# Optimization experiments

Measured on AMD Instinct MI355X. Metric: run time of the kernel, lower is better.

## Reference

```python
import jax, jax.numpy as jnp
import numpy as np

V = 30000
Y = 30000
D = 768
B = 8
N = 512
PAD_ID = 0
POS_EXPONENT = 1
NEG_INF = 1e12
LN_EPS = 1e-5


def setup_inputs() -> dict:
    key = jax.random.key(0)
    k1, k2, k3, k4, k5 = jax.random.split(key, 5)
    M_s = jax.random.randint(k1, (B, N), 0, V, dtype=jnp.int64)
    E_v = jax.random.normal(k2, (V, D), dtype=jnp.float32) * 0.02
    E_y = jax.random.normal(k3, (Y, D), dtype=jnp.float32) * 0.02
    # padding_idx=0 -> zero rows
    E_v = E_v.at[PAD_ID].set(0.0)
    E_y = E_y.at[PAD_ID].set(0.0)
    W_A = jax.random.normal(k4, (D, D), dtype=jnp.float32) * (1.0 / np.sqrt(D))
    W_O = jax.random.normal(k5, (D, D), dtype=jnp.float32) * (1.0 / np.sqrt(D))
    gamma = jnp.ones((D,), dtype=jnp.float32)
    beta = jnp.zeros((D,), dtype=jnp.float32)
    return {"M_s": M_s, "E_v": E_v, "E_y": E_y, "W_A": W_A, "W_O": W_O,
            "gamma": gamma, "beta": beta}


def positional_rep(seq_len: int, exponent: int) -> jnp.ndarray:
    idx = jnp.arange(seq_len)
    rel = (idx[None, :] - idx[:, None]).astype(jnp.float32)  # [N, N], j - i
    sign = jnp.where(rel >= 0, 1.0, -1.0)
    return sign * jnp.abs(rel) ** exponent


def layer_norm(x, gamma, beta):
    mu = jnp.mean(x, axis=-1, keepdims=True)
    var = jnp.mean((x - mu) ** 2, axis=-1, keepdims=True)
    return (x - mu) * jax.lax.rsqrt(var + LN_EPS) * gamma + beta


def reference(M_s, E_v, E_y, W_A, W_O, gamma, beta):
    # Embedding lookup (dropout is identity at eval / p=0)
    X = E_v[M_s]                                   # [B, N, D]
    Q = X                                          # self-attention mode (v_q=None)
    mask = (M_s != PAD_ID)                         # [B, N]

    # attention: logits = (Q @ W_A) @ X^T + pos_bias, mask, softmax
    logits = jnp.einsum('bnd,bmd->bnm', Q @ W_A, X)  # [B, N, N]
    logits = logits + positional_rep(X.shape[1], POS_EXPONENT)[None]
    logits = jnp.where(mask[:, None, :], logits, -NEG_INF)
    A = jax.nn.softmax(logits, axis=-1)            # [B, N, N]
    Q_c = jnp.einsum('bnm,bmd->bnd', A, X @ W_O)   # [B, N, D]

    H = layer_norm(Q_c + Q, gamma, beta)           # [B, N, D]
    y_logits = jnp.einsum('bnd,yd->bny', H, E_y)   # [B, N, Y]
    return y_logits, A
```

## Files before the change

### kernel.cpp

```cpp
#include <hip/hip_runtime.h>
#include <hip/hip_bf16.h>

using bf16 = __hip_bfloat16;
typedef __attribute__((ext_vector_type(8))) short bf16x8;
typedef __attribute__((ext_vector_type(4))) float f32x4;

#define DEV __device__ __forceinline__

#define AS1 __attribute__((address_space(1)))
#define AS3 __attribute__((address_space(3)))
#define SB  __builtin_amdgcn_sched_barrier(0)
#define BARR __builtin_amdgcn_s_barrier()
#define LG0 asm volatile("s_waitcnt lgkmcnt(0)" ::: "memory")
#define VM4 asm volatile("s_waitcnt vmcnt(4)" ::: "memory")
#define VM0 asm volatile("s_waitcnt vmcnt(0)" ::: "memory")

static constexpr int Bsz = 8, Nseq = 512, Dm = 768, Vv = 30000, Yv = 30000;
static constexpr int Ypad = 30208;
static constexpr int Tok = Bsz * Nseq;
static constexpr int NT = Dm / 64;

#define MF16(MQ, NQ)                                                          \
    __builtin_amdgcn_s_setprio(1);                                            \
    _Pragma("unroll") for (int mm = 0; mm < 4; ++mm)                          \
    _Pragma("unroll") for (int nn = 0; nn < 2; ++nn) {                        \
        acc[(MQ)*4+mm][(NQ)*2+nn] = __builtin_amdgcn_mfma_f32_16x16x32_bf16(  \
            afr[mm][0], bfr[nn][0], acc[(MQ)*4+mm][(NQ)*2+nn], 0, 0, 0);      \
        acc[(MQ)*4+mm][(NQ)*2+nn] = __builtin_amdgcn_mfma_f32_16x16x32_bf16(  \
            afr[mm][1], bfr[nn][1], acc[(MQ)*4+mm][(NQ)*2+nn], 0, 0, 0);      \
    }                                                                         \
    __builtin_amdgcn_s_setprio(0);

__global__ __launch_bounds__(512, 2)
void gemm_big(const bf16* __restrict__ Ag, const bf16* __restrict__ Bg,
              float* __restrict__ Cg)
{
    __shared__ bf16 sm[8][8192];

    int bid = blockIdx.x;
    { int cpx = gridDim.x >> 3; bid = (bid & 7) * cpx + (bid >> 3); }
    const int mTile = bid & 15;
    const int nTile = bid >> 4;

    const int tid  = threadIdx.x;
    const int lane = tid & 63;
    const int wid  = tid >> 6;
    const int wm   = wid >> 2;
    const int wn   = wid & 3;

    const int lr = tid >> 3;
    const int sc = ((tid & 7) ^ (lr & 7)) << 3;
    const bf16* aS = Ag + (long)(mTile * 256 + lr) * Dm + sc;
    const bf16* bS = Bg + (long)(nTile * 256 + lr) * Dm + sc;
    const int ldsOff = wid << 9;

    auto stage = [&](int ci, int op, int h, int tile) {
        const bf16* s = (op ? bS : aS) + (long)h * 128 * Dm + tile * 64;
        __builtin_amdgcn_global_load_lds((const AS1 void*)s,
            (AS3 void*)&sm[ci][ldsOff], 16, 0, 0);
        __builtin_amdgcn_global_load_lds((const AS1 void*)(s + (long)64 * Dm),
            (AS3 void*)&sm[ci][4096 + ldsOff], 16, 0, 0);
    };

    const int fl = lane & 15;
    const int fh = lane >> 4;
    const int e0 = (fh ^ (fl & 7)) << 3;
    const int aro = (wm * 64 + fl) * 64;
    const int bro = (wn * 32 + fl) * 64;

    f32x4 acc[8][4] = {};
    bf16x8 afr[4][2], bfr[2][2];

    auto rdA = [&](int ci) {
#pragma unroll
        for (int mm = 0; mm < 4; ++mm) {
            afr[mm][0] = *(const bf16x8*)&sm[ci][aro + mm * 1024 + e0];
            afr[mm][1] = *(const bf16x8*)&sm[ci][aro + mm * 1024 + (e0 ^ 32)];
        }
    };
    auto rdB = [&](int ci) {
#pragma unroll
        for (int nn = 0; nn < 2; ++nn) {
            bfr[nn][0] = *(const bf16x8*)&sm[ci][bro + nn * 1024 + e0];
            bfr[nn][1] = *(const bf16x8*)&sm[ci][bro + nn * 1024 + (e0 ^ 32)];
        }
    };

    stage(0, 0, 0, 0); stage(2, 1, 0, 0); stage(3, 1, 1, 0); stage(1, 0, 1, 0);
    stage(4, 0, 0, 1); stage(7, 1, 1, 1);
    VM4; SB; BARR; SB;

#pragma unroll 1
    for (int t = 0; t < NT - 2; t += 2) {
        stage(6, 1, 0, t + 1);
        rdA(0); rdB(2);
        SB; BARR; LG0; SB;
        MF16(0, 0)
        SB; BARR; SB;
        stage(5, 0, 1, t + 1);
        rdB(3);
        SB; BARR; LG0; SB;
        MF16(0, 1)
        SB; BARR; SB;
        stage(0, 0, 0, t + 2);
        rdA(1);
        SB; BARR; LG0; SB;
        MF16(1, 1)
        SB; BARR; SB;
        stage(3, 1, 1, t + 2);
        rdB(2);
        SB; BARR; LG0; SB;
        MF16(1, 0)
        VM4;
        SB; BARR; SB;
        stage(2, 1, 0, t + 2);
        rdA(4); rdB(6);
        SB; BARR; LG0; SB;
        MF16(0, 0)
        SB; BARR; SB;
        stage(1, 0, 1, t + 2);
        rdB(7);
        SB; BARR; LG0; SB;
        MF16(0, 1)
        SB; BARR; SB;
        stage(4, 0, 0, t + 3);
        rdA(5);
        SB; BARR; LG0; SB;
        MF16(1, 1)
        SB; BARR; SB;
        stage(7, 1, 1, t + 3);
        rdB(6);
        SB; BARR; LG0; SB;
        MF16(1, 0)
        VM4;
        SB; BARR; SB;
    }

    {
        const int t = NT - 2;
        stage(6, 1, 0, t + 1);
        rdA(0); rdB(2);
        SB; BARR; LG0; SB;
        MF16(0, 0)
        SB; BARR; SB;
        stage(5, 0, 1, t + 1);
        rdB(3);
        SB; BARR; LG0; SB;
        MF16(0, 1)
        SB; BARR; SB;
        rdA(1);
        SB; BARR; LG0; SB;
        MF16(1, 1)
        SB; BARR; SB;
        rdB(2);
        SB; BARR; LG0; SB;
        MF16(1, 0)
        VM0;
        SB; BARR; SB;
        rdA(4); rdB(6);
        SB; BARR; LG0; SB;
        MF16(0, 0)
        SB; BARR; SB;
        rdB(7);
        SB; BARR; LG0; SB;
        MF16(0, 1)
        SB; BARR; SB;
        rdA(5);
        SB; BARR; LG0; SB;
        MF16(1, 1)
        SB; BARR; SB;
        rdB(6);
        SB; BARR; LG0; SB;
        MF16(1, 0)
    }

    const int rB = mTile * 256 + wm * 64 + fh * 4;
    const int cB = nTile * 256 + wn * 32 + fl;
#pragma unroll
    for (int mq = 0; mq < 2; ++mq)
#pragma unroll
    for (int mm = 0; mm < 4; ++mm)
#pragma unroll
    for (int nq = 0; nq < 2; ++nq)
#pragma unroll
    for (int nn = 0; nn < 2; ++nn) {
        const int c = cB + nq * 128 + nn * 16;
        if (c >= Yv) continue;
        const int r = rB + mq * 128 + mm * 16;
#pragma unroll
        for (int j = 0; j < 4; ++j)
            Cg[(long)(r + j) * Yv + c] = acc[mq * 4 + mm][nq * 2 + nn][j];
    }
}

template<bool STORE_BF16>
__global__ __launch_bounds__(256)
void gemm_bt(const bf16* __restrict__ Ag, const bf16* __restrict__ Bg,
             void* __restrict__ Cg, int M, int Nc, int K, int ldc,
             long sA, long sB, long sC)
{
    __shared__ bf16 As[128 * 32];
    __shared__ bf16 Bs[128 * 32];

    const int bz = blockIdx.z;
    const bf16* A  = Ag + (long)bz * sA;
    const bf16* Bm = Bg + (long)bz * sB;

    const int bid = blockIdx.x;
    const int nTilesM = M >> 7;
    const int mTile = bid % nTilesM;
    const int nTile = bid / nTilesM;

    const int tid  = threadIdx.x;
    const int wave = tid >> 6;
    const int lane = tid & 63;

    const int sRow = (wave << 4) + (lane >> 2);
    const int sCol = (lane & 3) << 3;

    const long aBase = (long)(mTile * 128) * K;
    const long bBase = (long)(nTile * 128) * K;

    const int fl = lane & 15;
    const int fh = lane >> 4;
    const int wRow = (wave >> 1) << 6;
    const int wCol = (wave & 1) << 6;

    f32x4 acc[4][4] = {};

    for (int k0 = 0; k0 < K; k0 += 32) {
#pragma unroll
        for (int t = 0; t < 2; ++t) {
            const bf16* gA = A  + aBase + (long)(t * 64 + sRow) * K + (k0 + sCol);
            const bf16* gB = Bm + bBase + (long)(t * 64 + sRow) * K + (k0 + sCol);
            bf16* lA = &As[(t * 64 + (wave << 4)) * 32];
            bf16* lB = &Bs[(t * 64 + (wave << 4)) * 32];
            __builtin_amdgcn_global_load_lds(
                (const AS1 void*)gA, (AS3 void*)lA, 16, 0, 0);
            __builtin_amdgcn_global_load_lds(
                (const AS1 void*)gB, (AS3 void*)lB, 16, 0, 0);
        }
        __syncthreads();

        bf16x8 af[4], bfg[4];
#pragma unroll
        for (int m = 0; m < 4; ++m)
            af[m] = *(const bf16x8*)&As[(wRow + m * 16 + fl) * 32 + fh * 8];
#pragma unroll
        for (int n = 0; n < 4; ++n)
            bfg[n] = *(const bf16x8*)&Bs[(wCol + n * 16 + fl) * 32 + fh * 8];
#pragma unroll
        for (int m = 0; m < 4; ++m)
#pragma unroll
            for (int n = 0; n < 4; ++n)
                acc[m][n] = __builtin_amdgcn_mfma_f32_16x16x32_bf16(
                    af[m], bfg[n], acc[m][n], 0, 0, 0);
        __syncthreads();
    }

    const int rBase = mTile * 128 + wRow + fh * 4;
    const int cBase = nTile * 128 + wCol + fl;
#pragma unroll
    for (int m = 0; m < 4; ++m) {
#pragma unroll
        for (int n = 0; n < 4; ++n) {
            int gc = cBase + n * 16;
            int gr = rBase + m * 16;
            if (STORE_BF16) {
                bf16* C = (bf16*)Cg + (long)bz * sC;
#pragma unroll
                for (int j = 0; j < 4; ++j)
                    C[(long)(gr + j) * ldc + gc] = __float2bfloat16(acc[m][n][j]);
            } else {
                float* C = (float*)Cg + (long)bz * sC;
#pragma unroll
                for (int j = 0; j < 4; ++j)
                    C[(long)(gr + j) * ldc + gc] = acc[m][n][j];
            }
        }
    }
}

__global__ __launch_bounds__(192) void k_cvt_ey(const float* __restrict__ Ey,
                                                bf16* __restrict__ Eyb)
{
    int row = blockIdx.x;
    int d = threadIdx.x * 4;
    union { bf16 h[4]; uint2 u; } pk;
    if (row < Yv) {
        float4 v = *(const float4*)(Ey + (long)row * Dm + d);
        pk.h[0] = __float2bfloat16(v.x); pk.h[1] = __float2bfloat16(v.y);
        pk.h[2] = __float2bfloat16(v.z); pk.h[3] = __float2bfloat16(v.w);
    } else {
        pk.h[0] = pk.h[1] = pk.h[2] = pk.h[3] = __float2bfloat16(0.f);
    }
    *(uint2*)(Eyb + (long)row * Dm + d) = pk.u;
}

__global__ void k_wT(const float* __restrict__ WA, const float* __restrict__ WO,
                     bf16* __restrict__ WAT, bf16* __restrict__ WOT)
{
    __shared__ float t[32][33];
    const float* W = blockIdx.z ? WO : WA;
    bf16* WT = blockIdx.z ? WOT : WAT;
    int bx = blockIdx.x * 32;
    int by = blockIdx.y * 32;
    int tx = threadIdx.x, ty = threadIdx.y;
#pragma unroll
    for (int i = 0; i < 32; i += 8)
        t[ty + i][tx] = W[(long)(bx + ty + i) * Dm + (by + tx)];
    __syncthreads();
#pragma unroll
    for (int i = 0; i < 32; i += 8)
        WT[(long)(by + ty + i) * Dm + (bx + tx)] = __float2bfloat16(t[tx][ty + i]);
}

__global__ __launch_bounds__(192) void k_gather(const int* __restrict__ Ms,
                                                const float* __restrict__ Ev,
                                                bf16* __restrict__ Xb)
{
    int token = blockIdx.x;
    int id = Ms[token];
    int d = threadIdx.x * 4;
    float4 v = *(const float4*)(Ev + (long)id * Dm + d);
    union { bf16 h[4]; uint2 u; } pk;
    pk.h[0] = __float2bfloat16(v.x); pk.h[1] = __float2bfloat16(v.y);
    pk.h[2] = __float2bfloat16(v.z); pk.h[3] = __float2bfloat16(v.w);
    *(uint2*)(Xb + (long)token * Dm + d) = pk.u;
}

__global__ void k_xwoT(const bf16* __restrict__ Xo, bf16* __restrict__ XoT)
{
    __shared__ bf16 t[32][33];
    int b = blockIdx.z;
    const bf16* src = Xo + (long)b * Nseq * Dm;
    bf16* dst = XoT + (long)b * Dm * Nseq;
    int bx = blockIdx.x * 32;
    int by = blockIdx.y * 32;
    int tx = threadIdx.x, ty = threadIdx.y;
#pragma unroll
    for (int i = 0; i < 32; i += 8)
        t[ty + i][tx] = src[(long)(bx + ty + i) * Dm + (by + tx)];
    __syncthreads();
#pragma unroll
    for (int i = 0; i < 32; i += 8)
        dst[(long)(by + ty + i) * Nseq + (bx + tx)] = t[tx][ty + i];
}

DEV float waveMax(float v) {
#pragma unroll
    for (int o = 32; o > 0; o >>= 1) v = fmaxf(v, __shfl_xor(v, o, 64));
    return v;
}
DEV float waveSum(float v) {
#pragma unroll
    for (int o = 32; o > 0; o >>= 1) v += __shfl_xor(v, o, 64);
    return v;
}

__global__ __launch_bounds__(256) void k_softmax(const float* __restrict__ L,
                                                 const int* __restrict__ Ms,
                                                 float* __restrict__ Aout,
                                                 bf16* __restrict__ Ab)
{
    __shared__ float red[8];
    int row = blockIdx.x;
    int b = row >> 9, i = row & 511;
    const float* l = L + (long)row * Nseq;
    const int* ms = Ms + (b << 9);
    int t = threadIdx.x;
    int wid = t >> 6, lane = t & 63;
    int j0 = t, j1 = t + 256;

    float a0 = l[j0] + (float)(j0 - i);
    float a1 = l[j1] + (float)(j1 - i);
    if (ms[j0] == 0) a0 = -1e12f;
    if (ms[j1] == 0) a1 = -1e12f;

    float m = waveMax(fmaxf(a0, a1));
    if (lane == 0) red[wid] = m;
    __syncthreads();
    m = fmaxf(fmaxf(red[0], red[1]), fmaxf(red[2], red[3]));

    float e0 = expf(a0 - m), e1 = expf(a1 - m);
    float s = waveSum(e0 + e1);
    if (lane == 0) red[4 + wid] = s;
    __syncthreads();
    s = red[4] + red[5] + red[6] + red[7];
    float inv = 1.0f / s;

    float r0 = e0 * inv, r1 = e1 * inv;
    Aout[(long)row * Nseq + j0] = r0;
    Aout[(long)row * Nseq + j1] = r1;
    Ab[(long)row * Nseq + j0] = __float2bfloat16(r0);
    Ab[(long)row * Nseq + j1] = __float2bfloat16(r1);
}

__global__ __launch_bounds__(256) void k_ln(const float* __restrict__ Qc,
                                            const int* __restrict__ Ms,
                                            const float* __restrict__ Ev,
                                            const float* __restrict__ gamma,
                                            const float* __restrict__ beta,
                                            bf16* __restrict__ Hb)
{
    __shared__ float red[8];
    int row = blockIdx.x;
    int id = Ms[row];
    const float* q = Qc + (long)row * Dm;
    const float* e = Ev + (long)id * Dm;
    int t = threadIdx.x;
    int wid = t >> 6, lane = t & 63;

    float x[3];
#pragma unroll
    for (int c = 0; c < 3; ++c) x[c] = q[t + c * 256] + e[t + c * 256];

    float s = waveSum(x[0] + x[1] + x[2]);
    if (lane == 0) red[wid] = s;
    __syncthreads();
    float mu = (red[0] + red[1] + red[2] + red[3]) * (1.0f / 768.0f);

    float vs = 0.f;
#pragma unroll
    for (int c = 0; c < 3; ++c) { float d = x[c] - mu; vs += d * d; }
    vs = waveSum(vs);
    if (lane == 0) red[4 + wid] = vs;
    __syncthreads();
    float var = (red[4] + red[5] + red[6] + red[7]) * (1.0f / 768.0f);
    float rstd = rsqrtf(var + 1e-5f);

#pragma unroll
    for (int c = 0; c < 3; ++c) {
        int d = t + c * 256;
        Hb[(long)row * Dm + d] =
            __float2bfloat16((x[c] - mu) * rstd * gamma[d] + beta[d]);
    }
}

extern "C" void kernel_launch(void* const* d_in, const int* in_sizes, int n_in,
                              void* d_out, int out_size, void* d_ws, size_t ws_size,
                              hipStream_t stream)
{
    const int*   Ms    = (const int*)d_in[0];
    const float* Ev    = (const float*)d_in[1];
    const float* Ey    = (const float*)d_in[2];
    const float* WA    = (const float*)d_in[3];
    const float* WO    = (const float*)d_in[4];
    const float* gamma = (const float*)d_in[5];
    const float* beta  = (const float*)d_in[6];

    float* y_out = (float*)d_out;
    float* A_out = y_out + (size_t)Tok * Yv;

    char* ws = (char*)d_ws;
    size_t off = 0;
    auto alloc = [&](size_t n) { char* p = ws + off; off += (n + 255) & ~(size_t)255; return p; };
    bf16*  Xb    = (bf16*) alloc((size_t)Tok * Dm * 2);
    bf16*  WAbT  = (bf16*) alloc((size_t)Dm * Dm * 2);
    bf16*  WObT  = (bf16*) alloc((size_t)Dm * Dm * 2);
    bf16*  QWb   = (bf16*) alloc((size_t)Tok * Dm * 2);
    bf16*  XWob  = (bf16*) alloc((size_t)Tok * Dm * 2);
    bf16*  XWobT = (bf16*) alloc((size_t)Tok * Dm * 2);
    float* Lf    = (float*)alloc((size_t)Tok * Nseq * 4);
    bf16*  Ab    = (bf16*) alloc((size_t)Tok * Nseq * 2);
    float* Qc    = (float*)alloc((size_t)Tok * Dm * 4);
    bf16*  Hb    = (bf16*) alloc((size_t)Tok * Dm * 2);
    bf16*  Eyb   = (bf16*) alloc((size_t)Ypad * Dm * 2);

    k_cvt_ey<<<dim3(Ypad), dim3(192), 0, stream>>>(Ey, Eyb);
    k_wT<<<dim3(24, 24, 2), dim3(32, 8), 0, stream>>>(WA, WO, WAbT, WObT);
    k_gather<<<dim3(Tok), dim3(192), 0, stream>>>(Ms, Ev, Xb);
    gemm_bt<true><<<dim3(192), dim3(256), 0, stream>>>(
        Xb, WAbT, (void*)QWb, Tok, Dm, Dm, Dm, 0L, 0L, 0L);
    gemm_bt<true><<<dim3(192), dim3(256), 0, stream>>>(
        Xb, WObT, (void*)XWob, Tok, Dm, Dm, Dm, 0L, 0L, 0L);
    gemm_bt<false><<<dim3(16, 1, 8), dim3(256), 0, stream>>>(
        QWb, Xb, (void*)Lf, Nseq, Nseq, Dm, Nseq,
        (long)Nseq * Dm, (long)Nseq * Dm, (long)Nseq * Nseq);
    k_softmax<<<dim3(Tok), dim3(256), 0, stream>>>(Lf, Ms, A_out, Ab);
    k_xwoT<<<dim3(16, 24, 8), dim3(32, 8), 0, stream>>>(XWob, XWobT);
    gemm_bt<false><<<dim3(24, 1, 8), dim3(256), 0, stream>>>(
        Ab, XWobT, (void*)Qc, Nseq, Dm, Nseq, Dm,
        (long)Nseq * Nseq, (long)Dm * Nseq, (long)Nseq * Dm);
    k_ln<<<dim3(Tok), dim3(256), 0, stream>>>(Qc, Ms, Ev, gamma, beta, Hb);
    gemm_big<<<dim3(16 * (Ypad / 256)), dim3(512), 0, stream>>>(Hb, Eyb, y_out);
}
```

Before: 391.4 us.

## Make vocab GEMM persistent over N-tiles, double-buffer B fragments, fuse projection GEMMs

The large output GEMM now launches 256 persistent blocks. Each block keeps one M tile and loops over N tiles with a stride of 16, instead of launching one block per tile. It uses two B fragment register sets, so the fourth MFMA group reuses already-loaded B data and skips an LDS read. The two D×D projection GEMMs are merged into one GEMM against a concatenated weight matrix, and downstream kernels read the result through a new lda stride. This removes per-block launch and tail overhead plus a kernel launch, at the cost of more registers and possible load imbalance from the 118/16 tile split.

```diff
diff --git a/kernel.cpp b/kernel.cpp
--- a/kernel.cpp
+++ b/kernel.cpp
@@ -17,17 +17,18 @@
 
 static constexpr int Bsz = 8, Nseq = 512, Dm = 768, Vv = 30000, Yv = 30000;
 static constexpr int Ypad = 30208;
+static constexpr int NTILE = 118;
 static constexpr int Tok = Bsz * Nseq;
 static constexpr int NT = Dm / 64;
 
-#define MF16(MQ, NQ)                                                          \
+#define MF16(MQ, NQ, BR)                                                      \
     __builtin_amdgcn_s_setprio(1);                                            \
     _Pragma("unroll") for (int mm = 0; mm < 4; ++mm)                          \
     _Pragma("unroll") for (int nn = 0; nn < 2; ++nn) {                        \
         acc[(MQ)*4+mm][(NQ)*2+nn] = __builtin_amdgcn_mfma_f32_16x16x32_bf16(  \
-            afr[mm][0], bfr[nn][0], acc[(MQ)*4+mm][(NQ)*2+nn], 0, 0, 0);      \
+            afr[mm][0], BR[nn][0], acc[(MQ)*4+mm][(NQ)*2+nn], 0, 0, 0);       \
         acc[(MQ)*4+mm][(NQ)*2+nn] = __builtin_amdgcn_mfma_f32_16x16x32_bf16(  \
-            afr[mm][1], bfr[nn][1], acc[(MQ)*4+mm][(NQ)*2+nn], 0, 0, 0);      \
+            afr[mm][1], BR[nn][1], acc[(MQ)*4+mm][(NQ)*2+nn], 0, 0, 0);       \
     }                                                                         \
     __builtin_amdgcn_s_setprio(0);
 
@@ -37,10 +38,9 @@
 {
     __shared__ bf16 sm[8][8192];
 
-    int bid = blockIdx.x;
-    { int cpx = gridDim.x >> 3; bid = (bid & 7) * cpx + (bid >> 3); }
-    const int mTile = bid & 15;
-    const int nTile = bid >> 4;
+    const int b = blockIdx.x;
+    const int mTile = b >> 4;
+    const int sIdx  = b & 15;
 
     const int tid  = threadIdx.x;
     const int lane = tid & 63;
@@ -51,16 +51,7 @@
     const int lr = tid >> 3;
     const int sc = ((tid & 7) ^ (lr & 7)) << 3;
     const bf16* aS = Ag + (long)(mTile * 256 + lr) * Dm + sc;
-    const bf16* bS = Bg + (long)(nTile * 256 + lr) * Dm + sc;
     const int ldsOff = wid << 9;
-
-    auto stage = [&](int ci, int op, int h, int tile) {
-        const bf16* s = (op ? bS : aS) + (long)h * 128 * Dm + tile * 64;
-        __builtin_amdgcn_global_load_lds((const AS1 void*)s,
-            (AS3 void*)&sm[ci][ldsOff], 16, 0, 0);
-        __builtin_amdgcn_global_load_lds((const AS1 void*)(s + (long)64 * Dm),
-            (AS3 void*)&sm[ci][4096 + ldsOff], 16, 0, 0);
-    };
 
     const int fl = lane & 15;
     const int fh = lane >> 4;
@@ -68,135 +59,140 @@
     const int aro = (wm * 64 + fl) * 64;
     const int bro = (wn * 32 + fl) * 64;
 
-    f32x4 acc[8][4] = {};
-    bf16x8 afr[4][2], bfr[2][2];
-
-    auto rdA = [&](int ci) {
-#pragma unroll
-        for (int mm = 0; mm < 4; ++mm) {
-            afr[mm][0] = *(const bf16x8*)&sm[ci][aro + mm * 1024 + e0];
-            afr[mm][1] = *(const bf16x8*)&sm[ci][aro + mm * 1024 + (e0 ^ 32)];
+    bf16x8 afr[4][2], b0r[2][2], b1r[2][2];
+
+#define STAGE(CI, OP, H, TILE)                                                 \
+    {                                                                          \
+        const bf16* _s = ((OP) ? bS : aS) + (long)(H) * 128 * Dm + (TILE) * 64;\
+        __builtin_amdgcn_global_load_lds((const AS1 void*)_s,                  \
+            (AS3 void*)&sm[CI][ldsOff], 16, 0, 0);                             \
+        __builtin_amdgcn_global_load_lds((const AS1 void*)(_s + (long)64 * Dm),\
+            (AS3 void*)&sm[CI][4096 + ldsOff], 16, 0, 0);                      \
+    }
+#define RDA(CI)                                                                \
+    _Pragma("unroll") for (int mm = 0; mm < 4; ++mm) {                         \
+        afr[mm][0] = *(const bf16x8*)&sm[CI][aro + mm * 1024 + e0];            \
+        afr[mm][1] = *(const bf16x8*)&sm[CI][aro + mm * 1024 + (e0 ^ 32)];     \
+    }
+#define RDB(BR, CI)                                                            \
+    _Pragma("unroll") for (int nn = 0; nn < 2; ++nn) {                         \
+        BR[nn][0] = *(const bf16x8*)&sm[CI][bro + nn * 1024 + e0];             \
+        BR[nn][1] = *(const bf16x8*)&sm[CI][bro + nn * 1024 + (e0 ^ 32)];      \
+    }
+
+#pragma unroll 1
+    for (int nTile = sIdx; nTile < NTILE; nTile += 16) {
+        const bf16* bS = Bg + (long)(nTile * 256 + lr) * Dm + sc;
+        f32x4 acc[8][4] = {};
+
+        STAGE(0, 0, 0, 0) STAGE(2, 1, 0, 0) STAGE(3, 1, 1, 0) STAGE(1, 0, 1, 0)
+        STAGE(4, 0, 0, 1) STAGE(7, 1, 1, 1)
+        VM4; SB; BARR; SB;
+
+#pragma unroll 1
+        for (int t = 0; t < NT - 2; t += 2) {
+            STAGE(6, 1, 0, t + 1)
+            RDA(0) RDB(b0r, 2)
+            SB; BARR; LG0; SB;
+            MF16(0, 0, b0r)
+            SB; BARR; SB;
+            STAGE(5, 0, 1, t + 1)
+            RDB(b1r, 3)
+            SB; BARR; LG0; SB;
+            MF16(0, 1, b1r)
+            SB; BARR; SB;
+            STAGE(0, 0, 0, t + 2)
+            RDA(1)
+            SB; BARR; LG0; SB;
+            MF16(1, 1, b1r)
+            SB; BARR; SB;
+            STAGE(3, 1, 1, t + 2)
+            VM4; SB; BARR; SB;
+            MF16(1, 0, b0r)
+            SB; BARR; SB;
+            STAGE(2, 1, 0, t + 2)
+            RDA(4) RDB(b0r, 6)
+            SB; BARR; LG0; SB;
+            MF16(0, 0, b0r)
+            SB; BARR; SB;
+            STAGE(1, 0, 1, t + 2)
+            RDB(b1r, 7)
+            SB; BARR; LG0; SB;
+            MF16(0, 1, b1r)
+            SB; BARR; SB;
+            STAGE(4, 0, 0, t + 3)
+            RDA(5)
+            SB; BARR; LG0; SB;
+            MF16(1, 1, b1r)
+            SB; BARR; SB;
+            STAGE(7, 1, 1, t + 3)
+            VM4; SB; BARR; SB;
+            MF16(1, 0, b0r)
+            SB; BARR; SB;
         }
-    };
-    auto rdB = [&](int ci) {
+
+        {
+            const int t = NT - 2;
+            STAGE(6, 1, 0, t + 1)
+            RDA(0) RDB(b0r, 2)
+            SB; BARR; LG0; SB;
+            MF16(0, 0, b0r)
+            SB; BARR; SB;
+            STAGE(5, 0, 1, t + 1)
+            RDB(b1r, 3)
+            SB; BARR; LG0; SB;
+            MF16(0, 1, b1r)
+            SB; BARR; SB;
+            RDA(1)
+            SB; BARR; LG0; SB;
+            MF16(1, 1, b1r)
+            SB; BARR; SB;
+            VM0; SB; BARR; SB;
+            MF16(1, 0, b0r)
+            SB; BARR; SB;
+            RDA(4) RDB(b0r, 6)
+            SB; BARR; LG0; SB;
+            MF16(0, 0, b0r)
+            SB; BARR; SB;
+            RDB(b1r, 7)
+            SB; BARR; LG0; SB;
+            MF16(0, 1, b1r)
+            SB; BARR; SB;
+            RDA(5)
+            SB; BARR; LG0; SB;
+            MF16(1, 1, b1r)
+            SB; BARR; SB;
+            SB; BARR; SB;
+            MF16(1, 0, b0r)
+        }
+
+        const int rB = mTile * 256 + wm * 64 + fh * 4;
+        const int cB = nTile * 256 + wn * 32 + fl;
+#pragma unroll
+        for (int mq = 0; mq < 2; ++mq)
+#pragma unroll
+        for (int mm = 0; mm < 4; ++mm)
+#pragma unroll
+        for (int nq = 0; nq < 2; ++nq)
 #pragma unroll
         for (int nn = 0; nn < 2; ++nn) {
-            bfr[nn][0] = *(const bf16x8*)&sm[ci][bro + nn * 1024 + e0];
-            bfr[nn][1] = *(const bf16x8*)&sm[ci][bro + nn * 1024 + (e0 ^ 32)];
+            const int c = cB + nq * 128 + nn * 16;
+            if (c >= Yv) continue;
+            const int r = rB + mq * 128 + mm * 16;
+#pragma unroll
+            for (int j = 0; j < 4; ++j)
+                Cg[(long)(r + j) * Yv + c] = acc[mq * 4 + mm][nq * 2 + nn][j];
         }
-    };
-
-    stage(0, 0, 0, 0); stage(2, 1, 0, 0); stage(3, 1, 1, 0); stage(1, 0, 1, 0);
-    stage(4, 0, 0, 1); stage(7, 1, 1, 1);
-    VM4; SB; BARR; SB;
-
-#pragma unroll 1
-    for (int t = 0; t < NT - 2; t += 2) {
-        stage(6, 1, 0, t + 1);
-        rdA(0); rdB(2);
-        SB; BARR; LG0; SB;
-        MF16(0, 0)
-        SB; BARR; SB;
-        stage(5, 0, 1, t + 1);
-        rdB(3);
-        SB; BARR; LG0; SB;
-        MF16(0, 1)
-        SB; BARR; SB;
-        stage(0, 0, 0, t + 2);
-        rdA(1);
-        SB; BARR; LG0; SB;
-        MF16(1, 1)
-        SB; BARR; SB;
-        stage(3, 1, 1, t + 2);
-        rdB(2);
-        SB; BARR; LG0; SB;
-        MF16(1, 0)
-        VM4;
-        SB; BARR; SB;
-        stage(2, 1, 0, t + 2);
-        rdA(4); rdB(6);
-        SB; BARR; LG0; SB;
-        MF16(0, 0)
-        SB; BARR; SB;
-        stage(1, 0, 1, t + 2);
-        rdB(7);
-        SB; BARR; LG0; SB;
-        MF16(0, 1)
-        SB; BARR; SB;
-        stage(4, 0, 0, t + 3);
-        rdA(5);
-        SB; BARR; LG0; SB;
-        MF16(1, 1)
-        SB; BARR; SB;
-        stage(7, 1, 1, t + 3);
-        rdB(6);
-        SB; BARR; LG0; SB;
-        MF16(1, 0)
-        VM4;
-        SB; BARR; SB;
-    }
-
-    {
-        const int t = NT - 2;
-        stage(6, 1, 0, t + 1);
-        rdA(0); rdB(2);
-        SB; BARR; LG0; SB;
-        MF16(0, 0)
-        SB; BARR; SB;
-        stage(5, 0, 1, t + 1);
-        rdB(3);
-        SB; BARR; LG0; SB;
-        MF16(0, 1)
-        SB; BARR; SB;
-        rdA(1);
-        SB; BARR; LG0; SB;
-        MF16(1, 1)
-        SB; BARR; SB;
-        rdB(2);
-        SB; BARR; LG0; SB;
-        MF16(1, 0)
-        VM0;
-        SB; BARR; SB;
-        rdA(4); rdB(6);
-        SB; BARR; LG0; SB;
-        MF16(0, 0)
-        SB; BARR; SB;
-        rdB(7);
-        SB; BARR; LG0; SB;
-        MF16(0, 1)
-        SB; BARR; SB;
-        rdA(5);
-        SB; BARR; LG0; SB;
-        MF16(1, 1)
-        SB; BARR; SB;
-        rdB(6);
-        SB; BARR; LG0; SB;
-        MF16(1, 0)
-    }
-
-    const int rB = mTile * 256 + wm * 64 + fh * 4;
-    const int cB = nTile * 256 + wn * 32 + fl;
-#pragma unroll
-    for (int mq = 0; mq < 2; ++mq)
-#pragma unroll
-    for (int mm = 0; mm < 4; ++mm)
-#pragma unroll
-    for (int nq = 0; nq < 2; ++nq)
-#pragma unroll
-    for (int nn = 0; nn < 2; ++nn) {
-        const int c = cB + nq * 128 + nn * 16;
-        if (c >= Yv) continue;
-        const int r = rB + mq * 128 + mm * 16;
-#pragma unroll
-        for (int j = 0; j < 4; ++j)
-            Cg[(long)(r + j) * Yv + c] = acc[mq * 4 + mm][nq * 2 + nn][j];
-    }
+    }
+#undef STAGE
+#undef RDA
+#undef RDB
 }
 
 template<bool STORE_BF16>
 __global__ __launch_bounds__(256)
 void gemm_bt(const bf16* __restrict__ Ag, const bf16* __restrict__ Bg,
-             void* __restrict__ Cg, int M, int Nc, int K, int ldc,
+             void* __restrict__ Cg, int M, int Nc, int K, int lda, int ldc,
              long sA, long sB, long sC)
 {
     __shared__ bf16 As[128 * 32];
@@ -218,7 +214,7 @@
     const int sRow = (wave << 4) + (lane >> 2);
     const int sCol = (lane & 3) << 3;
 
-    const long aBase = (long)(mTile * 128) * K;
+    const long aBase = (long)(mTile * 128) * lda;
     const long bBase = (long)(nTile * 128) * K;
 
     const int fl = lane & 15;
@@ -231,7 +227,7 @@
     for (int k0 = 0; k0 < K; k0 += 32) {
 #pragma unroll
         for (int t = 0; t < 2; ++t) {
-            const bf16* gA = A  + aBase + (long)(t * 64 + sRow) * K + (k0 + sCol);
+            const bf16* gA = A  + aBase + (long)(t * 64 + sRow) * lda + (k0 + sCol);
             const bf16* gB = Bm + bBase + (long)(t * 64 + sRow) * K + (k0 + sCol);
             bf16* lA = &As[(t * 64 + (wave << 4)) * 32];
             bf16* lB = &Bs[(t * 64 + (wave << 4)) * 32];
@@ -298,11 +294,11 @@
 }
 
 __global__ void k_wT(const float* __restrict__ WA, const float* __restrict__ WO,
-                     bf16* __restrict__ WAT, bf16* __restrict__ WOT)
+                     bf16* __restrict__ Wcat)
 {
     __shared__ float t[32][33];
     const float* W = blockIdx.z ? WO : WA;
-    bf16* WT = blockIdx.z ? WOT : WAT;
+    bf16* WT = Wcat + (size_t)blockIdx.z * Dm * Dm;
     int bx = blockIdx.x * 32;
     int by = blockIdx.y * 32;
     int tx = threadIdx.x, ty = threadIdx.y;
@@ -333,14 +329,14 @@
 {
     __shared__ bf16 t[32][33];
     int b = blockIdx.z;
-    const bf16* src = Xo + (long)b * Nseq * Dm;
+    const bf16* src = Xo + (long)b * Nseq * 1536 + 768;
     bf16* dst = XoT + (long)b * Dm * Nseq;
     int bx = blockIdx.x * 32;
     int by = blockIdx.y * 32;
     int tx = threadIdx.x, ty = threadIdx.y;
 #pragma unroll
     for (int i = 0; i < 32; i += 8)
-        t[ty + i][tx] = src[(long)(bx + ty + i) * Dm + (by + tx)];
+        t[ty + i][tx] = src[(long)(bx + ty + i) * 1536 + (by + tx)];
     __syncthreads();
 #pragma unroll
     for (int i = 0; i < 32; i += 8)
@@ -456,10 +452,8 @@
     size_t off = 0;
     auto alloc = [&](size_t n) { char* p = ws + off; off += (n + 255) & ~(size_t)255; return p; };
     bf16*  Xb    = (bf16*) alloc((size_t)Tok * Dm * 2);
-    bf16*  WAbT  = (bf16*) alloc((size_t)Dm * Dm * 2);
-    bf16*  WObT  = (bf16*) alloc((size_t)Dm * Dm * 2);
-    bf16*  QWb   = (bf16*) alloc((size_t)Tok * Dm * 2);
-    bf16*  XWob  = (bf16*) alloc((size_t)Tok * Dm * 2);
+    bf16*  WcatT = (bf16*) alloc((size_t)2 * Dm * Dm * 2);
+    bf16*  QXWb  = (bf16*) alloc((size_t)Tok * 1536 * 2);
     bf16*  XWobT = (bf16*) alloc((size_t)Tok * Dm * 2);
     float* Lf    = (float*)alloc((size_t)Tok * Nseq * 4);
     bf16*  Ab    = (bf16*) alloc((size_t)Tok * Nseq * 2);
@@ -468,20 +462,18 @@
     bf16*  Eyb   = (bf16*) alloc((size_t)Ypad * Dm * 2);
 
     k_cvt_ey<<<dim3(Ypad), dim3(192), 0, stream>>>(Ey, Eyb);
-    k_wT<<<dim3(24, 24, 2), dim3(32, 8), 0, stream>>>(WA, WO, WAbT, WObT);
+    k_wT<<<dim3(24, 24, 2), dim3(32, 8), 0, stream>>>(WA, WO, WcatT);
     k_gather<<<dim3(Tok), dim3(192), 0, stream>>>(Ms, Ev, Xb);
-    gemm_bt<true><<<dim3(192), dim3(256), 0, stream>>>(
-        Xb, WAbT, (void*)QWb, Tok, Dm, Dm, Dm, 0L, 0L, 0L);
-    gemm_bt<true><<<dim3(192), dim3(256), 0, stream>>>(
-        Xb, WObT, (void*)XWob, Tok, Dm, Dm, Dm, 0L, 0L, 0L);
+    gemm_bt<true><<<dim3(384), dim3(256), 0, stream>>>(
+        Xb, WcatT, (void*)QXWb, Tok, 1536, Dm, Dm, 1536, 0L, 0L, 0L);
     gemm_bt<false><<<dim3(16, 1, 8), dim3(256), 0, stream>>>(
-        QWb, Xb, (void*)Lf, Nseq, Nseq, Dm, Nseq,
-        (long)Nseq * Dm, (long)Nseq * Dm, (long)Nseq * Nseq);
+        QXWb, Xb, (void*)Lf, Nseq, Nseq, Dm, 1536, Nseq,
+        (long)Nseq * 1536, (long)Nseq * Dm, (long)Nseq * Nseq);
     k_softmax<<<dim3(Tok), dim3(256), 0, stream>>>(Lf, Ms, A_out, Ab);
-    k_xwoT<<<dim3(16, 24, 8), dim3(32, 8), 0, stream>>>(XWob, XWobT);
+    k_xwoT<<<dim3(16, 24, 8), dim3(32, 8), 0, stream>>>(QXWb, XWobT);
     gemm_bt<false><<<dim3(24, 1, 8), dim3(256), 0, stream>>>(
-        Ab, XWobT, (void*)Qc, Nseq, Dm, Nseq, Dm,
+        Ab, XWobT, (void*)Qc, Nseq, Dm, Nseq, Nseq, Dm,
         (long)Nseq * Nseq, (long)Dm * Nseq, (long)Nseq * Dm);
     k_ln<<<dim3(Tok), dim3(256), 0, stream>>>(Qc, Ms, Ev, gamma, beta, Hb);
-    gemm_big<<<dim3(16 * (Ypad / 256)), dim3(512), 0, stream>>>(Hb, Eyb, y_out);
-}
+    gemm_big<<<dim3(256), dim3(512), 0, stream>>>(Hb, Eyb, y_out);
+}
```

New measurement: 447.0 us. 1.14x slower.
